# Optimization experiments

Hardware: AMD Instinct MI355X
Metric: run time of the kernel (lower is better)

The kernel has to match this reference:

```python
import jax, jax.numpy as jnp
from jax import lax
import numpy as np

N_E = 1024
E_DIM = 512
BETA = 0.25


def setup_inputs() -> dict:
    key = jax.random.key(0)
    k1, k2 = jax.random.split(key)
    z = jax.random.normal(k1, (16, 4096, E_DIM), dtype=jnp.float32)
    # torch init: uniform(-1/n_e, 1/n_e)
    codebook = jax.random.uniform(k2, (N_E, E_DIM), dtype=jnp.float32,
                                  minval=-1.0 / N_E, maxval=1.0 / N_E)
    return {"z": z, "codebook": codebook}


def reference(z, codebook):
    zf = z.reshape(-1, z.shape[-1])                      # (N, e_dim)
    # squared-distance matrix: ||z||^2 + ||e||^2 - 2 z e^T  -> (N, n_e)
    d = (jnp.sum(zf * zf, axis=1, keepdims=True)
         + jnp.sum(codebook * codebook, axis=1)
         - 2.0 * (zf @ codebook.T))
    idx = jnp.argmin(d, axis=1)                          # (N,)
    z_q = codebook[idx].reshape(z.shape)                 # (B, S, e_dim)
    loss = (jnp.mean((z_q - lax.stop_gradient(z)) ** 2)
            + BETA * jnp.mean((lax.stop_gradient(z_q) - z) ** 2))
    # straight-through estimator
    z_q_st = z + lax.stop_gradient(z_q - z)
    # perplexity of code usage (mean of one-hot == normalized counts)
    counts = jnp.zeros((codebook.shape[0],), dtype=z.dtype).at[idx].add(1.0)
    e_mean = counts / idx.shape[0]
    perplexity = jnp.exp(-jnp.sum(e_mean * jnp.log(e_mean + 1e-10)))
    return (loss, z_q_st, idx, perplexity)
```

## Files before the change

### kernel.cpp

```cpp
#include <hip/hip_runtime.h>
#include <hip/hip_bf16.h>

#define N_ROWS 65536
#define EDIM   512
#define NCODES 1024

#define WS_LOSS   0
#define WS_COUNTS 1
#define WS_ENORM  1025
#define WS_ZNORM  2049
#define WS_AMBCNT (2049 + 65536)
#define WS_WINNER (WS_AMBCNT + 1)
#define WS_AMBLST (WS_WINNER + 65536)
#define AMB_CAP   32768
#define WS_E2_OFF (1u << 20)
#define WS_FAST_BYTES (3u * 1024u * 1024u + 4096u)

#define AMB_EPS 1.6e-4f

typedef short short8 __attribute__((ext_vector_type(8)));
typedef float f32x4  __attribute__((ext_vector_type(4)));

#define AS1C(p) ((const __attribute__((address_space(1))) void*)(p))
#define AS3(p)  ((__attribute__((address_space(3))) void*)(p))

static __device__ __forceinline__ unsigned short f2bf(float f) {
    unsigned u = __float_as_uint(f);
    u += 0x7FFFu + ((u >> 16) & 1u);
    return (unsigned short)(u >> 16);
}
static __device__ __forceinline__ float bf2f(unsigned short h) {
    return __uint_as_float(((unsigned)h) << 16);
}

__global__ __launch_bounds__(256) void vq_prep(const float* __restrict__ cb,
                                               float* __restrict__ ws) {
    int j = blockIdx.x;
    int tid = threadIdx.x;
    float2 v = *(const float2*)&cb[(size_t)j * EDIM + tid * 2];
    float s = v.x * v.x + v.y * v.y;
    #pragma unroll
    for (int off = 32; off > 0; off >>= 1) s += __shfl_down(s, off);
    __shared__ float ls[4];
    int wave = tid >> 6, lane = tid & 63;
    if (lane == 0) ls[wave] = s;
    __syncthreads();
    if (tid == 0) {
        ws[WS_ENORM + j] = ls[0] + ls[1] + ls[2] + ls[3];
        ws[WS_COUNTS + j] = 0.0f;
        if (j == 0) {
            ws[WS_LOSS] = 0.0f;
            ((int*)ws)[WS_AMBCNT] = 0;
        }
    }
}

__global__ __launch_bounds__(256) void vq_znorm(const float* __restrict__ z,
                                                float* __restrict__ ws) {
    int tid  = threadIdx.x;
    int lrow = tid >> 5;
    int c    = tid & 31;
    long row = (long)blockIdx.x * 8 + lrow;
    const float* p = z + row * EDIM + (c >> 3) * 128 + (c & 7);
    float r = p[0] * p[0];
    #pragma unroll
    for (int i = 1; i < 16; ++i) {
        float v = p[i * 8];
        r += v * v;
    }
    r += __shfl_xor(r, 1);
    r += __shfl_xor(r, 2);
    r += __shfl_xor(r, 4);
    r += __shfl_xor(r, 8);
    r += __shfl_xor(r, 16);
    if (c == 0) ws[WS_ZNORM + row] = r;
}

__global__ __launch_bounds__(256) void vq_convz(const float* __restrict__ z,
                                                unsigned short* __restrict__ z2) {
    const int tid = threadIdx.x;
    const int p = blockIdx.x;
    const long row0 = (long)p * 128;
    const int row = tid >> 1, half = tid & 1;
    for (int kc = 0; kc < 16; ++kc) {
        const float* src = z + (row0 + row) * EDIM + kc * 32 + half * 16;
        float f[16];
        #pragma unroll
        for (int q = 0; q < 4; ++q) {
            float4 v = ((const float4*)src)[q];
            f[q*4+0] = v.x; f[q*4+1] = v.y; f[q*4+2] = v.z; f[q*4+3] = v.w;
        }
        unsigned hi[8], lo[8];
        #pragma unroll
        for (int q = 0; q < 8; ++q) {
            unsigned short h0 = f2bf(f[2*q]);
            unsigned short h1 = f2bf(f[2*q+1]);
            unsigned short l0 = f2bf(f[2*q]   - bf2f(h0));
            unsigned short l1 = f2bf(f[2*q+1] - bf2f(h1));
            hi[q] = (unsigned)h0 | ((unsigned)h1 << 16);
            lo[q] = (unsigned)l0 | ((unsigned)l1 << 16);
        }
        size_t base = ((size_t)(p * 16 + kc) * 2) * 4096;
        unsigned* dhi = (unsigned*)(z2 + base        + row * 32 + half * 16);
        unsigned* dlo = (unsigned*)(z2 + base + 4096 + row * 32 + half * 16);
        ((uint4*)dhi)[0] = make_uint4(hi[0], hi[1], hi[2], hi[3]);
        ((uint4*)dhi)[1] = make_uint4(hi[4], hi[5], hi[6], hi[7]);
        ((uint4*)dlo)[0] = make_uint4(lo[0], lo[1], lo[2], lo[3]);
        ((uint4*)dlo)[1] = make_uint4(lo[4], lo[5], lo[6], lo[7]);
    }
}

__global__ __launch_bounds__(256) void vq_convcb(const float* __restrict__ cb,
                                                 unsigned short* __restrict__ e2) {
    const int tid = threadIdx.x;
    const int cc = blockIdx.x;
    const int row = tid >> 1, half = tid & 1;
    for (int kc = 0; kc < 16; ++kc) {
        const float* src = cb + (size_t)(cc * 128 + row) * EDIM + kc * 32 + half * 16;
        float f[16];
        #pragma unroll
        for (int q = 0; q < 4; ++q) {
            float4 v = ((const float4*)src)[q];
            f[q*4+0] = v.x; f[q*4+1] = v.y; f[q*4+2] = v.z; f[q*4+3] = v.w;
        }
        unsigned hi[8], lo[8];
        #pragma unroll
        for (int q = 0; q < 8; ++q) {
            unsigned short h0 = f2bf(f[2*q]);
            unsigned short h1 = f2bf(f[2*q+1]);
            unsigned short l0 = f2bf(f[2*q]   - bf2f(h0));
            unsigned short l1 = f2bf(f[2*q+1] - bf2f(h1));
            hi[q] = (unsigned)h0 | ((unsigned)h1 << 16);
            lo[q] = (unsigned)l0 | ((unsigned)l1 << 16);
        }
        size_t base = ((size_t)(cc * 16 + kc) * 2) * 4096;
        unsigned* dhi = (unsigned*)(e2 + base        + row * 32 + half * 16);
        unsigned* dlo = (unsigned*)(e2 + base + 4096 + row * 32 + half * 16);
        ((uint4*)dhi)[0] = make_uint4(hi[0], hi[1], hi[2], hi[3]);
        ((uint4*)dhi)[1] = make_uint4(hi[4], hi[5], hi[6], hi[7]);
        ((uint4*)dlo)[0] = make_uint4(lo[0], lo[1], lo[2], lo[3]);
        ((uint4*)dlo)[1] = make_uint4(lo[4], lo[5], lo[6], lo[7]);
    }
}

__global__ __launch_bounds__(256, 2) void vq_mfma(const unsigned short* __restrict__ z2,
                                                  const unsigned short* __restrict__ e2,
                                                  const float* __restrict__ ws,
                                                  int* __restrict__ winner,
                                                  int* __restrict__ amb_count,
                                                  int* __restrict__ amb_list) {
    __shared__ unsigned short stage[16384];
    __shared__ float fv1[2][128];
    __shared__ float fv2[2][128];
    __shared__ int   fc1[2][128];

    const int tid = threadIdx.x;
    const int lane = tid & 63, w = tid >> 6;
    const int rw = (w & 1) * 64, cw = (w >> 1) * 64;
    const int ml = lane & 15, kg = lane >> 4;
    const long row0 = (long)blockIdx.x * 128;
    const float* __restrict__ enorm = ws + WS_ENORM;

    float v1[16], v2[16];
    int   c1[16];
    #pragma unroll
    for (int i = 0; i < 16; ++i) { v1[i] = INFINITY; v2[i] = INFINITY; c1[i] = 0; }

    const unsigned short* zt = stage;
    const unsigned short* et = stage + 8192;

    for (int cc = 0; cc < 8; ++cc) {
        f32x4 acc[4][4];
        #pragma unroll
        for (int rt = 0; rt < 4; ++rt)
            #pragma unroll
            for (int ct = 0; ct < 4; ++ct)
                acc[rt][ct] = (f32x4){0.f, 0.f, 0.f, 0.f};

        for (int kc = 0; kc < 16; ++kc) {
            __syncthreads();
            const uint4* zsrc = (const uint4*)(z2 + (size_t)(blockIdx.x * 16 + kc) * 8192);
            const uint4* esrc = (const uint4*)(e2 + (size_t)(cc * 16 + kc) * 8192);
            uint4* st = (uint4*)stage;
#if defined(__has_builtin) && __has_builtin(__builtin_amdgcn_global_load_lds)
            #pragma unroll
            for (int it = 0; it < 4; ++it) {
                int base = it * 256 + w * 64;
                __builtin_amdgcn_global_load_lds(AS1C(zsrc + base + lane), AS3(st + base), 16, 0, 0);
            }
            #pragma unroll
            for (int it = 0; it < 4; ++it) {
                int base = it * 256 + w * 64;
                __builtin_amdgcn_global_load_lds(AS1C(esrc + base + lane), AS3(st + 1024 + base), 16, 0, 0);
            }
#else
            #pragma unroll
            for (int it = 0; it < 4; ++it) {
                int i = it * 256 + tid;
                st[i] = zsrc[i];
            }
            #pragma unroll
            for (int it = 0; it < 4; ++it) {
                int i = it * 256 + tid;
                st[1024 + i] = esrc[i];
            }
#endif
            __syncthreads();

            short8 a[4][2], b[4][2];
            #pragma unroll
            for (int rt = 0; rt < 4; ++rt) {
                a[rt][0] = *(const short8*)&zt[        (rw + rt * 16 + ml) * 32 + kg * 8];
                a[rt][1] = *(const short8*)&zt[4096 + (rw + rt * 16 + ml) * 32 + kg * 8];
            }
            #pragma unroll
            for (int ct = 0; ct < 4; ++ct) {
                b[ct][0] = *(const short8*)&et[        (cw + ct * 16 + ml) * 32 + kg * 8];
                b[ct][1] = *(const short8*)&et[4096 + (cw + ct * 16 + ml) * 32 + kg * 8];
            }
            #pragma unroll
            for (int rt = 0; rt < 4; ++rt)
                #pragma unroll
                for (int ct = 0; ct < 4; ++ct) {
                    acc[rt][ct] = __builtin_amdgcn_mfma_f32_16x16x32_bf16(a[rt][0], b[ct][0], acc[rt][ct], 0, 0, 0);
                    acc[rt][ct] = __builtin_amdgcn_mfma_f32_16x16x32_bf16(a[rt][0], b[ct][1], acc[rt][ct], 0, 0, 0);
                    acc[rt][ct] = __builtin_amdgcn_mfma_f32_16x16x32_bf16(a[rt][1], b[ct][0], acc[rt][ct], 0, 0, 0);
                }
        }

        float en[4];
        #pragma unroll
        for (int ct = 0; ct < 4; ++ct) en[ct] = enorm[cc * 128 + cw + ct * 16 + ml];
        #pragma unroll
        for (int rt = 0; rt < 4; ++rt)
            #pragma unroll
            for (int ct = 0; ct < 4; ++ct) {
                int code = cc * 128 + cw + ct * 16 + ml;
                #pragma unroll
                for (int reg = 0; reg < 4; ++reg) {
                    float d = fmaf(-2.0f, acc[rt][ct][reg], en[ct]);
                    int i = rt * 4 + reg;
                    bool lt1 = d < v1[i];
                    bool lt2 = d < v2[i];
                    v2[i] = lt1 ? v1[i] : (lt2 ? d : v2[i]);
                    v1[i] = lt1 ? d : v1[i];
                    c1[i] = lt1 ? code : c1[i];
                }
            }
    }

    #pragma unroll
    for (int i = 0; i < 16; ++i) {
        #pragma unroll
        for (int off = 1; off < 16; off <<= 1) {
            float ov1 = __shfl_xor(v1[i], off);
            int   oc1 = __shfl_xor(c1[i], off);
            float ov2 = __shfl_xor(v2[i], off);
            bool take = (ov1 < v1[i]) || (ov1 == v1[i] && oc1 < c1[i]);
            float nv2 = take ? fminf(v1[i], ov2) : fminf(v2[i], ov1);
            v1[i] = take ? ov1 : v1[i];
            c1[i] = take ? oc1 : c1[i];
            v2[i] = nv2;
        }
    }
    __syncthreads();
    if (ml == 0) {
        #pragma unroll
        for (int i = 0; i < 16; ++i) {
            int row = rw + (i >> 2) * 16 + kg * 4 + (i & 3);
            fv1[w >> 1][row] = v1[i];
            fv2[w >> 1][row] = v2[i];
            fc1[w >> 1][row] = c1[i];
        }
    }
    __syncthreads();
    if (tid < 128) {
        float a1 = fv1[0][tid], a2 = fv2[0][tid];
        int   ac = fc1[0][tid];
        float b1 = fv1[1][tid], b2 = fv2[1][tid];
        int   bc = fc1[1][tid];
        bool take = (b1 < a1) || (b1 == a1 && bc < ac);
        float V1 = take ? b1 : a1;
        int   C1 = take ? bc : ac;
        float V2 = take ? fminf(a1, b2) : fminf(a2, b1);
        winner[row0 + tid] = C1;
        if (V2 - V1 < AMB_EPS) {
            int p = atomicAdd(amb_count, 1);
            if (p < AMB_CAP) amb_list[p] = (int)(row0 + tid);
        }
    }
}

#define RB 8
#define ZSR 9
__global__ __launch_bounds__(256) void vq_recheck(const float* __restrict__ z,
                                                  const float* __restrict__ cb,
                                                  const float* __restrict__ ws,
                                                  int* __restrict__ winner,
                                                  const int* __restrict__ amb_count,
                                                  const int* __restrict__ amb_list) {
    __shared__ float zs[EDIM * ZSR];
    __shared__ float wred_d[4];
    __shared__ int   wred_i[4];
    const int tid = threadIdx.x;
    const int lane = tid & 63, wv = tid >> 6;
    const float* __restrict__ enorm = ws + WS_ENORM;

    int n = *amb_count;
    bool overflow = (n > AMB_CAP);
    if (overflow) n = N_ROWS;
    int nIter = (n + RB - 1) / RB;

    const float* ec[4];
    float en4[4];
    #pragma unroll
    for (int c = 0; c < 4; ++c) {
        ec[c]  = cb + (size_t)(tid + 256 * c) * EDIM;
        en4[c] = enorm[tid + 256 * c];
    }

    for (int ii = blockIdx.x; ii < nIter; ii += gridDim.x) {
        int rows[RB];
        #pragma unroll
        for (int j = 0; j < RB; ++j) {
            int idx = ii * RB + j;
            if (idx >= n) idx = n - 1;
            rows[j] = overflow ? idx : amb_list[idx];
        }
        __syncthreads();
        #pragma unroll
        for (int j = 0; j < RB; ++j) {
            float2 v = *(const float2*)&z[(long)rows[j] * EDIM + tid * 2];
            zs[(tid * 2 + 0) * ZSR + j] = v.x;
            zs[(tid * 2 + 1) * ZSR + j] = v.y;
        }
        __syncthreads();

        float acc[RB][4];
        #pragma unroll
        for (int r = 0; r < RB; ++r)
            #pragma unroll
            for (int c = 0; c < 4; ++c) acc[r][c] = 0.0f;

        for (int k0 = 0; k0 < EDIM; k0 += 32) {
            float ain[RB][4];
            #pragma unroll
            for (int r = 0; r < RB; ++r)
                #pragma unroll
                for (int c = 0; c < 4; ++c) ain[r][c] = 0.0f;
            #pragma unroll
            for (int ks = 0; ks < 32; ks += 8) {
                float er[4][8];
                #pragma unroll
                for (int c = 0; c < 4; ++c) {
                    float4 a = *(const float4*)&ec[c][k0 + ks];
                    float4 b = *(const float4*)&ec[c][k0 + ks + 4];
                    er[c][0]=a.x; er[c][1]=a.y; er[c][2]=a.z; er[c][3]=a.w;
                    er[c][4]=b.x; er[c][5]=b.y; er[c][6]=b.z; er[c][7]=b.w;
                }
                #pragma unroll
                for (int kk = 0; kk < 8; ++kk) {
                    const float* zp = &zs[(k0 + ks + kk) * ZSR];
                    float4 z0 = *(const float4*)zp;
                    float4 z1 = *(const float4*)(zp + 4);
                    float zr[RB] = {z0.x, z0.y, z0.z, z0.w, z1.x, z1.y, z1.z, z1.w};
                    #pragma unroll
                    for (int r = 0; r < RB; ++r)
                        #pragma unroll
                        for (int c = 0; c < 4; ++c)
                            ain[r][c] = fmaf(zr[r], er[c][kk], ain[r][c]);
                }
            }
            #pragma unroll
            for (int r = 0; r < RB; ++r)
                #pragma unroll
                for (int c = 0; c < 4; ++c) acc[r][c] += ain[r][c];
        }

        #pragma unroll
        for (int r = 0; r < RB; ++r) {
            float zn = ws[WS_ZNORM + rows[r]];
            float bd = INFINITY;
            int   bc = 0;
            #pragma unroll
            for (int c = 0; c < 4; ++c) {
                float t = zn + en4[c];
                float d = t - 2.0f * acc[r][c];
                if (d < bd) { bd = d; bc = tid + 256 * c; }
            }
            #pragma unroll
            for (int off = 1; off < 64; off <<= 1) {
                float od = __shfl_xor(bd, off);
                int   oi = __shfl_xor(bc, off);
                if (od < bd || (od == bd && oi < bc)) { bd = od; bc = oi; }
            }
            if (lane == 0) { wred_d[wv] = bd; wred_i[wv] = bc; }
            __syncthreads();
            if (tid == 0) {
                float fd = wred_d[0]; int fi = wred_i[0];
                #pragma unroll
                for (int t2 = 1; t2 < 4; ++t2) {
                    if (wred_d[t2] < fd || (wred_d[t2] == fd && wred_i[t2] < fi)) {
                        fd = wred_d[t2]; fi = wred_i[t2];
                    }
                }
                winner[rows[r]] = fi;
            }
            __syncthreads();
        }
    }
}

__global__ __launch_bounds__(256) void vq_emit(const float* __restrict__ z,
                                               const float* __restrict__ cb,
                                               const int* __restrict__ winner,
                                               float* __restrict__ ws,
                                               float* __restrict__ out_zq,
                                               float* __restrict__ out_idx) {
    __shared__ float lred[4];
    const int tid = threadIdx.x;
    const long row0 = (long)blockIdx.x * 128;
    if (tid < 128) {
        int wi = winner[row0 + tid];
        out_idx[row0 + tid] = (float)wi;
        atomicAdd(&ws[WS_COUNTS + wi], 1.0f);
    }
    float lsum = 0.0f;
    for (int r = 0; r < 128; ++r) {
        int wv = winner[row0 + r];
        float2 e  = *(const float2*)&cb[(size_t)wv * EDIM + tid * 2];
        float2 zz = *(const float2*)&z[(row0 + r) * EDIM + tid * 2];
        float d0 = e.x - zz.x, d1 = e.y - zz.y;
        float2 o; o.x = zz.x + d0; o.y = zz.y + d1;
        *(float2*)&out_zq[(row0 + r) * EDIM + tid * 2] = o;
        lsum = fmaf(d0, d0, fmaf(d1, d1, lsum));
    }
    #pragma unroll
    for (int off = 32; off > 0; off >>= 1) lsum += __shfl_down(lsum, off);
    int wave = tid >> 6, lane = tid & 63;
    if (lane == 0) lred[wave] = lsum;
    __syncthreads();
    if (tid == 0) atomicAdd(&ws[WS_LOSS], lred[0] + lred[1] + lred[2] + lred[3]);
}

__global__ __launch_bounds__(1024) void vq_final(const float* __restrict__ ws,
                                                 float* __restrict__ out,
                                                 long off_perp) {
    int tid = threadIdx.x;
    float c = ws[WS_COUNTS + tid] * (1.0f / (float)N_ROWS);
    float t = c * logf(c + 1e-10f);
    #pragma unroll
    for (int off = 32; off > 0; off >>= 1) t += __shfl_down(t, off);
    __shared__ float ls[16];
    int wave = tid >> 6, lane = tid & 63;
    if (lane == 0) ls[wave] = t;
    __syncthreads();
    if (tid == 0) {
        float h = 0.0f;
        #pragma unroll
        for (int i = 0; i < 16; ++i) h += ls[i];
        out[off_perp] = expf(-h);
        out[0] = ws[WS_LOSS] * 1.25f / (float)((long)N_ROWS * EDIM);
    }
}

#define ROWS_PER_BLOCK 128
#define CODE_CHUNK     64
#define KCHUNK         32
#define ZSTRIDE        132
#define ESTRIDE        68

__global__ __launch_bounds__(256) void vq_main_fb(const float* __restrict__ z,
                                                  const float* __restrict__ cb,
                                                  float* __restrict__ ws,
                                                  float* __restrict__ out_zq,
                                                  float* __restrict__ out_idx) {
    __shared__ float zt[KCHUNK * ZSTRIDE];
    __shared__ float et[KCHUNK * ESTRIDE];
    __shared__ float red_d[ROWS_PER_BLOCK * 8];
    __shared__ int   red_i[ROWS_PER_BLOCK * 8];
    __shared__ int   winner[ROWS_PER_BLOCK];
    __shared__ float lred[4];

    const int tid = threadIdx.x;
    const int tx = tid & 7;
    const int ty = tid >> 3;
    const long row0 = (long)blockIdx.x * ROWS_PER_BLOCK;
    const float* __restrict__ enorm = ws + WS_ENORM;
    const float* __restrict__ znorm = ws + WS_ZNORM;

    float zn[4];
    #pragma unroll
    for (int i = 0; i < 4; ++i) zn[i] = znorm[row0 + ty * 4 + i];

    float best[4];
    int   bidx[4];
    #pragma unroll
    for (int i = 0; i < 4; ++i) { best[i] = INFINITY; bidx[i] = 0; }

    const int kq    = (tid & 7) * 4;
    const int rbase = tid >> 3;

    for (int c = 0; c < NCODES; c += CODE_CHUNK) {
        float acc[4][8];
        #pragma unroll
        for (int i = 0; i < 4; ++i)
            #pragma unroll
            for (int j = 0; j < 8; ++j) acc[i][j] = 0.0f;

        for (int k0 = 0; k0 < EDIM; k0 += KCHUNK) {
            __syncthreads();
            #pragma unroll
            for (int it = 0; it < 4; ++it) {
                int r = rbase + it * 32;
                float4 v = *(const float4*)&z[(row0 + r) * EDIM + k0 + kq];
                zt[(kq + 0) * ZSTRIDE + r] = v.x;
                zt[(kq + 1) * ZSTRIDE + r] = v.y;
                zt[(kq + 2) * ZSTRIDE + r] = v.z;
                zt[(kq + 3) * ZSTRIDE + r] = v.w;
            }
            #pragma unroll
            for (int it = 0; it < 2; ++it) {
                int e = rbase + it * 32;
                float4 v = *(const float4*)&cb[(size_t)(c + e) * EDIM + k0 + kq];
                et[(kq + 0) * ESTRIDE + e] = v.x;
                et[(kq + 1) * ESTRIDE + e] = v.y;
                et[(kq + 2) * ESTRIDE + e] = v.z;
                et[(kq + 3) * ESTRIDE + e] = v.w;
            }
            __syncthreads();
            float ain[4][8];
            #pragma unroll
            for (int i = 0; i < 4; ++i)
                #pragma unroll
                for (int j = 0; j < 8; ++j) ain[i][j] = 0.0f;
            #pragma unroll
            for (int kk = 0; kk < KCHUNK; ++kk) {
                float4 zv = *(const float4*)&zt[kk * ZSTRIDE + ty * 4];
                float4 e0 = *(const float4*)&et[kk * ESTRIDE + tx * 8];
                float4 e1 = *(const float4*)&et[kk * ESTRIDE + tx * 8 + 4];
                float za[4] = {zv.x, zv.y, zv.z, zv.w};
                float ea[8] = {e0.x, e0.y, e0.z, e0.w, e1.x, e1.y, e1.z, e1.w};
                #pragma unroll
                for (int i = 0; i < 4; ++i)
                    #pragma unroll
                    for (int j = 0; j < 8; ++j)
                        ain[i][j] = fmaf(za[i], ea[j], ain[i][j]);
            }
            #pragma unroll
            for (int i = 0; i < 4; ++i)
                #pragma unroll
                for (int j = 0; j < 8; ++j) acc[i][j] += ain[i][j];
        }
        #pragma unroll
        for (int j = 0; j < 8; ++j) {
            int code = c + tx * 8 + j;
            float en = enorm[code];
            #pragma unroll
            for (int i = 0; i < 4; ++i) {
                float t = zn[i] + en;
                float d = t - 2.0f * acc[i][j];
                if (d < best[i]) { best[i] = d; bidx[i] = code; }
            }
        }
    }

    __syncthreads();
    #pragma unroll
    for (int i = 0; i < 4; ++i) {
        red_d[(ty * 4 + i) * 8 + tx] = best[i];
        red_i[(ty * 4 + i) * 8 + tx] = bidx[i];
    }
    __syncthreads();
    if (tid < ROWS_PER_BLOCK) {
        float bd = red_d[tid * 8];
        int   bi = red_i[tid * 8];
        #pragma unroll
        for (int t = 1; t < 8; ++t) {
            float dv = red_d[tid * 8 + t];
            int   iv = red_i[tid * 8 + t];
            if (dv < bd || (dv == bd && iv < bi)) { bd = dv; bi = iv; }
        }
        winner[tid] = bi;
        out_idx[row0 + tid] = (float)bi;
        atomicAdd(&ws[WS_COUNTS + bi], 1.0f);
    }
    __syncthreads();

    float lsum = 0.0f;
    for (int r = 0; r < ROWS_PER_BLOCK; ++r) {
        int w = winner[r];
        float2 e  = *(const float2*)&cb[(size_t)w * EDIM + tid * 2];
        float2 zz = *(const float2*)&z[(row0 + r) * EDIM + tid * 2];
        float d0 = e.x - zz.x, d1 = e.y - zz.y;
        float2 o; o.x = zz.x + d0; o.y = zz.y + d1;
        *(float2*)&out_zq[(row0 + r) * EDIM + tid * 2] = o;
        lsum = fmaf(d0, d0, fmaf(d1, d1, lsum));
    }
    #pragma unroll
    for (int off = 32; off > 0; off >>= 1) lsum += __shfl_down(lsum, off);
    int wave = tid >> 6, lane = tid & 63;
    if (lane == 0) lred[wave] = lsum;
    __syncthreads();
    if (tid == 0) atomicAdd(&ws[WS_LOSS], lred[0] + lred[1] + lred[2] + lred[3]);
}

extern "C" void kernel_launch(void* const* d_in, const int* in_sizes, int n_in,
                              void* d_out, int out_size, void* d_ws, size_t ws_size,
                              hipStream_t stream) {
    const float* z  = (const float*)d_in[0];
    const float* cb = (const float*)d_in[1];
    float* out = (float*)d_out;
    float* ws  = (float*)d_ws;

    float* out_zq  = out + 1;
    float* out_idx = out + 1 + (long)N_ROWS * EDIM;
    long   off_perp = 1 + (long)N_ROWS * EDIM + N_ROWS;

    hipLaunchKernelGGL(vq_prep, dim3(NCODES), dim3(256), 0, stream, cb, ws);
    hipLaunchKernelGGL(vq_znorm, dim3(N_ROWS / 8), dim3(256), 0, stream, z, ws);

    if (ws_size >= (size_t)WS_FAST_BYTES) {
        unsigned short* z2 = (unsigned short*)(out + 4);
        unsigned short* e2 = (unsigned short*)((char*)d_ws + WS_E2_OFF);
        int* winner    = ((int*)ws) + WS_WINNER;
        int* amb_count = ((int*)ws) + WS_AMBCNT;
        int* amb_list  = ((int*)ws) + WS_AMBLST;

        hipLaunchKernelGGL(vq_convz, dim3(N_ROWS / 128), dim3(256), 0, stream, z, z2);
        hipLaunchKernelGGL(vq_convcb, dim3(8), dim3(256), 0, stream, cb, e2);
        hipLaunchKernelGGL(vq_mfma, dim3(N_ROWS / 128), dim3(256), 0, stream,
                           z2, e2, ws, winner, amb_count, amb_list);
        hipLaunchKernelGGL(vq_recheck, dim3(512), dim3(256), 0, stream,
                           z, cb, ws, winner, amb_count, amb_list);
        hipLaunchKernelGGL(vq_emit, dim3(N_ROWS / 128), dim3(256), 0, stream,
                           z, cb, winner, ws, out_zq, out_idx);
    } else {
        hipLaunchKernelGGL(vq_main_fb, dim3(N_ROWS / 128), dim3(256), 0, stream,
                           z, cb, ws, out_zq, out_idx);
    }
    hipLaunchKernelGGL(vq_final, dim3(1), dim3(1024), 0, stream, ws, out, off_perp);
}
```

Baseline: 696.9 us.

## Double-buffer MFMA tiles with 512-thread blocks covering 256 codes per pass

```diff
diff --git a/kernel.cpp b/kernel.cpp
--- a/kernel.cpp
+++ b/kernel.cpp
@@ -143,33 +143,56 @@
     }
 }
 
-__global__ __launch_bounds__(256, 2) void vq_mfma(const unsigned short* __restrict__ z2,
+__device__ __forceinline__ void stage48(const char* zs, const char* es0, const char* es1,
+                                        char* db, int tid, int w) {
+    const int t16 = tid << 4;
+    const int wb  = w << 10;
+    __builtin_amdgcn_global_load_lds(AS1C(zs + t16),         AS3(db + wb),          16, 0, 0);
+    __builtin_amdgcn_global_load_lds(AS1C(zs + 8192 + t16),  AS3(db + 8192 + wb),   16, 0, 0);
+    __builtin_amdgcn_global_load_lds(AS1C(es0 + t16),        AS3(db + 16384 + wb),  16, 0, 0);
+    __builtin_amdgcn_global_load_lds(AS1C(es0 + 8192 + t16), AS3(db + 24576 + wb),  16, 0, 0);
+    __builtin_amdgcn_global_load_lds(AS1C(es1 + t16),        AS3(db + 32768 + wb),  16, 0, 0);
+    __builtin_amdgcn_global_load_lds(AS1C(es1 + 8192 + t16), AS3(db + 40960 + wb),  16, 0, 0);
+}
+
+__global__ __launch_bounds__(512, 2) void vq_mfma(const unsigned short* __restrict__ z2,
                                                   const unsigned short* __restrict__ e2,
                                                   const float* __restrict__ ws,
                                                   int* __restrict__ winner,
                                                   int* __restrict__ amb_count,
                                                   int* __restrict__ amb_list) {
-    __shared__ unsigned short stage[16384];
-    __shared__ float fv1[2][128];
-    __shared__ float fv2[2][128];
-    __shared__ int   fc1[2][128];
-
-    const int tid = threadIdx.x;
+    __shared__ __attribute__((aligned(16))) char sb[2][49152];
+    __shared__ float enorm_lds[NCODES];
+    __shared__ float fv1[4][128];
+    __shared__ float fv2[4][128];
+    __shared__ int   fc1[4][128];
+
+    const int tid  = threadIdx.x;
     const int lane = tid & 63, w = tid >> 6;
-    const int rw = (w & 1) * 64, cw = (w >> 1) * 64;
+    const int rw   = (w & 1) * 64;
+    const int wcol = w >> 1;
+    const int cw   = wcol * 64;
     const int ml = lane & 15, kg = lane >> 4;
     const long row0 = (long)blockIdx.x * 128;
-    const float* __restrict__ enorm = ws + WS_ENORM;
+
+    enorm_lds[tid]       = ws[WS_ENORM + tid];
+    enorm_lds[tid + 512] = ws[WS_ENORM + tid + 512];
 
     float v1[16], v2[16];
     int   c1[16];
     #pragma unroll
     for (int i = 0; i < 16; ++i) { v1[i] = INFINITY; v2[i] = INFINITY; c1[i] = 0; }
 
-    const unsigned short* zt = stage;
-    const unsigned short* et = stage + 8192;
-
-    for (int cc = 0; cc < 8; ++cc) {
+    const size_t zpan = (size_t)blockIdx.x * 16 * 8192;
+
+    stage48((const char*)(z2 + zpan),
+            (const char*)e2,
+            (const char*)(e2 + (size_t)16 * 8192),
+            sb[0], tid, w);
+    __syncthreads();
+
+    int cur = 0;
+    for (int p = 0; p < 4; ++p) {
         f32x4 acc[4][4];
         #pragma unroll
         for (int rt = 0; rt < 4; ++rt)
@@ -177,36 +200,18 @@
             for (int ct = 0; ct < 4; ++ct)
                 acc[rt][ct] = (f32x4){0.f, 0.f, 0.f, 0.f};
 
+        #pragma unroll 2
         for (int kc = 0; kc < 16; ++kc) {
-            __syncthreads();
-            const uint4* zsrc = (const uint4*)(z2 + (size_t)(blockIdx.x * 16 + kc) * 8192);
-            const uint4* esrc = (const uint4*)(e2 + (size_t)(cc * 16 + kc) * 8192);
-            uint4* st = (uint4*)stage;
-#if defined(__has_builtin) && __has_builtin(__builtin_amdgcn_global_load_lds)
-            #pragma unroll
-            for (int it = 0; it < 4; ++it) {
-                int base = it * 256 + w * 64;
-                __builtin_amdgcn_global_load_lds(AS1C(zsrc + base + lane), AS3(st + base), 16, 0, 0);
-            }
-            #pragma unroll
-            for (int it = 0; it < 4; ++it) {
-                int base = it * 256 + w * 64;
-                __builtin_amdgcn_global_load_lds(AS1C(esrc + base + lane), AS3(st + 1024 + base), 16, 0, 0);
-            }
-#else
-            #pragma unroll
-            for (int it = 0; it < 4; ++it) {
-                int i = it * 256 + tid;
-                st[i] = zsrc[i];
-            }
-            #pragma unroll
-            for (int it = 0; it < 4; ++it) {
-                int i = it * 256 + tid;
-                st[1024 + i] = esrc[i];
-            }
-#endif
-            __syncthreads();
-
+            const int s = p * 16 + kc;
+            if (s + 1 < 64) {
+                const int s2 = s + 1, p2 = s2 >> 4, kc2 = s2 & 15;
+                const char* zs  = (const char*)(z2 + zpan + (size_t)kc2 * 8192);
+                const char* es0 = (const char*)(e2 + ((size_t)(2 * p2)     * 16 + kc2) * 8192);
+                const char* es1 = (const char*)(e2 + ((size_t)(2 * p2 + 1) * 16 + kc2) * 8192);
+                stage48(zs, es0, es1, sb[cur ^ 1], tid, w);
+            }
+            const unsigned short* zt = (const unsigned short*)sb[cur];
+            const unsigned short* et = (const unsigned short*)(sb[cur] + 16384);
             short8 a[4][2], b[4][2];
             #pragma unroll
             for (int rt = 0; rt < 4; ++rt) {
@@ -215,8 +220,10 @@
             }
             #pragma unroll
             for (int ct = 0; ct < 4; ++ct) {
-                b[ct][0] = *(const short8*)&et[        (cw + ct * 16 + ml) * 32 + kg * 8];
-                b[ct][1] = *(const short8*)&et[4096 + (cw + ct * 16 + ml) * 32 + kg * 8];
+                const int c2  = cw + ct * 16 + ml;
+                const int off = (c2 >> 7) * 8192 + (c2 & 127) * 32 + kg * 8;
+                b[ct][0] = *(const short8*)&et[off];
+                b[ct][1] = *(const short8*)&et[off + 4096];
             }
             #pragma unroll
             for (int rt = 0; rt < 4; ++rt)
@@ -226,19 +233,21 @@
                     acc[rt][ct] = __builtin_amdgcn_mfma_f32_16x16x32_bf16(a[rt][0], b[ct][1], acc[rt][ct], 0, 0, 0);
                     acc[rt][ct] = __builtin_amdgcn_mfma_f32_16x16x32_bf16(a[rt][1], b[ct][0], acc[rt][ct], 0, 0, 0);
                 }
-        }
-
-        float en[4];
-        #pragma unroll
-        for (int ct = 0; ct < 4; ++ct) en[ct] = enorm[cc * 128 + cw + ct * 16 + ml];
-        #pragma unroll
-        for (int rt = 0; rt < 4; ++rt)
-            #pragma unroll
-            for (int ct = 0; ct < 4; ++ct) {
-                int code = cc * 128 + cw + ct * 16 + ml;
+            asm volatile("s_waitcnt vmcnt(0)" ::: "memory");
+            __builtin_amdgcn_s_barrier();
+            asm volatile("" ::: "memory");
+            cur ^= 1;
+        }
+
+        #pragma unroll
+        for (int ct = 0; ct < 4; ++ct) {
+            const int code = p * 256 + cw + ct * 16 + ml;
+            const float en = enorm_lds[code];
+            #pragma unroll
+            for (int rt = 0; rt < 4; ++rt)
                 #pragma unroll
                 for (int reg = 0; reg < 4; ++reg) {
-                    float d = fmaf(-2.0f, acc[rt][ct][reg], en[ct]);
+                    float d = fmaf(-2.0f, acc[rt][ct][reg], en);
                     int i = rt * 4 + reg;
                     bool lt1 = d < v1[i];
                     bool lt2 = d < v2[i];
@@ -246,7 +255,7 @@
                     v1[i] = lt1 ? d : v1[i];
                     c1[i] = lt1 ? code : c1[i];
                 }
-            }
+        }
     }
 
     #pragma unroll
@@ -268,25 +277,29 @@
         #pragma unroll
         for (int i = 0; i < 16; ++i) {
             int row = rw + (i >> 2) * 16 + kg * 4 + (i & 3);
-            fv1[w >> 1][row] = v1[i];
-            fv2[w >> 1][row] = v2[i];
-            fc1[w >> 1][row] = c1[i];
+            fv1[wcol][row] = v1[i];
+            fv2[wcol][row] = v2[i];
+            fc1[wcol][row] = c1[i];
         }
     }
     __syncthreads();
     if (tid < 128) {
-        float a1 = fv1[0][tid], a2 = fv2[0][tid];
-        int   ac = fc1[0][tid];
-        float b1 = fv1[1][tid], b2 = fv2[1][tid];
-        int   bc = fc1[1][tid];
-        bool take = (b1 < a1) || (b1 == a1 && bc < ac);
-        float V1 = take ? b1 : a1;
-        int   C1 = take ? bc : ac;
-        float V2 = take ? fminf(a1, b2) : fminf(a2, b1);
+        float V1 = fv1[0][tid], V2 = fv2[0][tid];
+        int   C1 = fc1[0][tid];
+        #pragma unroll
+        for (int g = 1; g < 4; ++g) {
+            float b1 = fv1[g][tid], b2 = fv2[g][tid];
+            int   bc = fc1[g][tid];
+            bool take = (b1 < V1) || (b1 == V1 && bc < C1);
+            float nv2 = take ? fminf(V1, b2) : fminf(V2, b1);
+            V1 = take ? b1 : V1;
+            C1 = take ? bc : C1;
+            V2 = nv2;
+        }
         winner[row0 + tid] = C1;
         if (V2 - V1 < AMB_EPS) {
-            int p = atomicAdd(amb_count, 1);
-            if (p < AMB_CAP) amb_list[p] = (int)(row0 + tid);
+            int pq = atomicAdd(amb_count, 1);
+            if (pq < AMB_CAP) amb_list[pq] = (int)(row0 + tid);
         }
     }
 }
@@ -629,7 +642,7 @@
 
         hipLaunchKernelGGL(vq_convz, dim3(N_ROWS / 128), dim3(256), 0, stream, z, z2);
         hipLaunchKernelGGL(vq_convcb, dim3(8), dim3(256), 0, stream, cb, e2);
-        hipLaunchKernelGGL(vq_mfma, dim3(N_ROWS / 128), dim3(256), 0, stream,
+        hipLaunchKernelGGL(vq_mfma, dim3(N_ROWS / 128), dim3(512), 0, stream,
                            z2, e2, ws, winner, amb_count, amb_list);
         hipLaunchKernelGGL(vq_recheck, dim3(512), dim3(256), 0, stream,
                            z, cb, ws, winner, amb_count, amb_list);
```

New measurement: 749.4 us. 7.5% more time.

## Double-buffer swizzled LDS staging in the MFMA distance kernel

Applied to the files above, without the earlier changes.

```diff
diff --git a/kernel.cpp b/kernel.cpp
--- a/kernel.cpp
+++ b/kernel.cpp
@@ -143,110 +143,128 @@
     }
 }
 
+__device__ __forceinline__ void stage32(const char* zs, const char* es,
+                                        char* db, int goff, int w) {
+    const int wb = w << 10;
+    #pragma unroll
+    for (int i = 0; i < 4; ++i) {
+        __builtin_amdgcn_global_load_lds(AS1C(zs + goff + i * 2048),
+                                         AS3(db + i * 4096 + wb), 16, 0, 0);
+        __builtin_amdgcn_global_load_lds(AS1C(es + goff + i * 2048),
+                                         AS3(db + 16384 + i * 4096 + wb), 16, 0, 0);
+    }
+}
+
 __global__ __launch_bounds__(256, 2) void vq_mfma(const unsigned short* __restrict__ z2,
                                                   const unsigned short* __restrict__ e2,
                                                   const float* __restrict__ ws,
                                                   int* __restrict__ winner,
                                                   int* __restrict__ amb_count,
                                                   int* __restrict__ amb_list) {
-    __shared__ unsigned short stage[16384];
+    __shared__ __attribute__((aligned(16))) char sb[2][32768];
+    __shared__ float enorm_lds[NCODES];
     __shared__ float fv1[2][128];
     __shared__ float fv2[2][128];
     __shared__ int   fc1[2][128];
 
-    const int tid = threadIdx.x;
+    const int tid  = threadIdx.x;
     const int lane = tid & 63, w = tid >> 6;
-    const int rw = (w & 1) * 64, cw = (w >> 1) * 64;
+    const int rw   = (w & 1) * 64;
+    const int wcol = w >> 1;
+    const int cw   = wcol * 64;
     const int ml = lane & 15, kg = lane >> 4;
     const long row0 = (long)blockIdx.x * 128;
-    const float* __restrict__ enorm = ws + WS_ENORM;
+
+    const int t3 = tid >> 3;
+    const int sl = (tid & 7) ^ (t3 & 7);
+    const int goff = t3 * 64 + (sl & 3) * 16 + (sl >> 2) * 8192;
+
+    const int xr = ml & 7;
+    const int o0 = (kg ^ xr) * 16;
+    const int o1 = ((4 + kg) ^ xr) * 16;
+    const int za = (rw + ml) * 128;
+    const int ea = 16384 + (cw + ml) * 128;
+
+    #pragma unroll
+    for (int i = 0; i < 4; ++i) enorm_lds[tid + i * 256] = ws[WS_ENORM + tid + i * 256];
 
     float v1[16], v2[16];
     int   c1[16];
     #pragma unroll
     for (int i = 0; i < 16; ++i) { v1[i] = INFINITY; v2[i] = INFINITY; c1[i] = 0; }
 
-    const unsigned short* zt = stage;
-    const unsigned short* et = stage + 8192;
-
-    for (int cc = 0; cc < 8; ++cc) {
-        f32x4 acc[4][4];
+    const char* z2b = (const char*)z2 + (size_t)blockIdx.x * 16 * 16384;
+    const char* e2b = (const char*)e2;
+
+    f32x4 acc[4][4];
+    #pragma unroll
+    for (int rt = 0; rt < 4; ++rt)
+        #pragma unroll
+        for (int ct = 0; ct < 4; ++ct)
+            acc[rt][ct] = (f32x4){0.f, 0.f, 0.f, 0.f};
+
+    stage32(z2b, e2b, sb[0], goff, w);
+    __syncthreads();
+
+    int cur = 0;
+    #pragma unroll 2
+    for (int s = 0; s < 128; ++s) {
+        if (s + 1 < 128) {
+            const int s2 = s + 1;
+            stage32(z2b + (size_t)(s2 & 15) * 16384,
+                    e2b + (size_t)s2 * 16384,
+                    sb[cur ^ 1], goff, w);
+        }
+        const char* bz = sb[cur];
+        short8 a[4][2], b[4][2];
+        #pragma unroll
+        for (int rt = 0; rt < 4; ++rt) {
+            a[rt][0] = *(const short8*)(bz + za + rt * 2048 + o0);
+            a[rt][1] = *(const short8*)(bz + za + rt * 2048 + o1);
+        }
+        #pragma unroll
+        for (int ct = 0; ct < 4; ++ct) {
+            b[ct][0] = *(const short8*)(bz + ea + ct * 2048 + o0);
+            b[ct][1] = *(const short8*)(bz + ea + ct * 2048 + o1);
+        }
         #pragma unroll
         for (int rt = 0; rt < 4; ++rt)
             #pragma unroll
-            for (int ct = 0; ct < 4; ++ct)
-                acc[rt][ct] = (f32x4){0.f, 0.f, 0.f, 0.f};
-
-        for (int kc = 0; kc < 16; ++kc) {
-            __syncthreads();
-            const uint4* zsrc = (const uint4*)(z2 + (size_t)(blockIdx.x * 16 + kc) * 8192);
-            const uint4* esrc = (const uint4*)(e2 + (size_t)(cc * 16 + kc) * 8192);
-            uint4* st = (uint4*)stage;
-#if defined(__has_builtin) && __has_builtin(__builtin_amdgcn_global_load_lds)
-            #pragma unroll
-            for (int it = 0; it < 4; ++it) {
-                int base = it * 256 + w * 64;
-                __builtin_amdgcn_global_load_lds(AS1C(zsrc + base + lane), AS3(st + base), 16, 0, 0);
-            }
-            #pragma unroll
-            for (int it = 0; it < 4; ++it) {
-                int base = it * 256 + w * 64;
-                __builtin_amdgcn_global_load_lds(AS1C(esrc + base + lane), AS3(st + 1024 + base), 16, 0, 0);
-            }
-#else
-            #pragma unroll
-            for (int it = 0; it < 4; ++it) {
-                int i = it * 256 + tid;
-                st[i] = zsrc[i];
-            }
-            #pragma unroll
-            for (int it = 0; it < 4; ++it) {
-                int i = it * 256 + tid;
-                st[1024 + i] = esrc[i];
-            }
-#endif
-            __syncthreads();
-
-            short8 a[4][2], b[4][2];
-            #pragma unroll
-            for (int rt = 0; rt < 4; ++rt) {
-                a[rt][0] = *(const short8*)&zt[        (rw + rt * 16 + ml) * 32 + kg * 8];
-                a[rt][1] = *(const short8*)&zt[4096 + (rw + rt * 16 + ml) * 32 + kg * 8];
-            }
-            #pragma unroll
             for (int ct = 0; ct < 4; ++ct) {
-                b[ct][0] = *(const short8*)&et[        (cw + ct * 16 + ml) * 32 + kg * 8];
-                b[ct][1] = *(const short8*)&et[4096 + (cw + ct * 16 + ml) * 32 + kg * 8];
+                acc[rt][ct] = __builtin_amdgcn_mfma_f32_16x16x32_bf16(a[rt][0], b[ct][0], acc[rt][ct], 0, 0, 0);
+                acc[rt][ct] = __builtin_amdgcn_mfma_f32_16x16x32_bf16(a[rt][0], b[ct][1], acc[rt][ct], 0, 0, 0);
+                acc[rt][ct] = __builtin_amdgcn_mfma_f32_16x16x32_bf16(a[rt][1], b[ct][0], acc[rt][ct], 0, 0, 0);
+            }
+        asm volatile("s_waitcnt vmcnt(0)" ::: "memory");
+        __builtin_amdgcn_s_barrier();
+        asm volatile("" ::: "memory");
+        cur ^= 1;
+
+        if ((s & 15) == 15) {
+            const int cc = s >> 4;
+            #pragma unroll
+            for (int ct = 0; ct < 4; ++ct) {
+                const int code = cc * 128 + cw + ct * 16 + ml;
+                const float en = enorm_lds[code];
+                #pragma unroll
+                for (int rt = 0; rt < 4; ++rt)
+                    #pragma unroll
+                    for (int reg = 0; reg < 4; ++reg) {
+                        float d = fmaf(-2.0f, acc[rt][ct][reg], en);
+                        int i = rt * 4 + reg;
+                        bool lt1 = d < v1[i];
+                        bool lt2 = d < v2[i];
+                        v2[i] = lt1 ? v1[i] : (lt2 ? d : v2[i]);
+                        v1[i] = lt1 ? d : v1[i];
+                        c1[i] = lt1 ? code : c1[i];
+                    }
             }
             #pragma unroll
             for (int rt = 0; rt < 4; ++rt)
                 #pragma unroll
-                for (int ct = 0; ct < 4; ++ct) {
-                    acc[rt][ct] = __builtin_amdgcn_mfma_f32_16x16x32_bf16(a[rt][0], b[ct][0], acc[rt][ct], 0, 0, 0);
-                    acc[rt][ct] = __builtin_amdgcn_mfma_f32_16x16x32_bf16(a[rt][0], b[ct][1], acc[rt][ct], 0, 0, 0);
-                    acc[rt][ct] = __builtin_amdgcn_mfma_f32_16x16x32_bf16(a[rt][1], b[ct][0], acc[rt][ct], 0, 0, 0);
-                }
-        }
-
-        float en[4];
-        #pragma unroll
-        for (int ct = 0; ct < 4; ++ct) en[ct] = enorm[cc * 128 + cw + ct * 16 + ml];
-        #pragma unroll
-        for (int rt = 0; rt < 4; ++rt)
-            #pragma unroll
-            for (int ct = 0; ct < 4; ++ct) {
-                int code = cc * 128 + cw + ct * 16 + ml;
-                #pragma unroll
-                for (int reg = 0; reg < 4; ++reg) {
-                    float d = fmaf(-2.0f, acc[rt][ct][reg], en[ct]);
-                    int i = rt * 4 + reg;
-                    bool lt1 = d < v1[i];
-                    bool lt2 = d < v2[i];
-                    v2[i] = lt1 ? v1[i] : (lt2 ? d : v2[i]);
-                    v1[i] = lt1 ? d : v1[i];
-                    c1[i] = lt1 ? code : c1[i];
-                }
-            }
+                for (int ct = 0; ct < 4; ++ct)
+                    acc[rt][ct] = (f32x4){0.f, 0.f, 0.f, 0.f};
+        }
     }
 
     #pragma unroll
@@ -268,9 +286,9 @@
         #pragma unroll
         for (int i = 0; i < 16; ++i) {
             int row = rw + (i >> 2) * 16 + kg * 4 + (i & 3);
-            fv1[w >> 1][row] = v1[i];
-            fv2[w >> 1][row] = v2[i];
-            fc1[w >> 1][row] = c1[i];
+            fv1[wcol][row] = v1[i];
+            fv2[wcol][row] = v2[i];
+            fc1[wcol][row] = c1[i];
         }
     }
     __syncthreads();
@@ -631,7 +649,7 @@
         hipLaunchKernelGGL(vq_convcb, dim3(8), dim3(256), 0, stream, cb, e2);
         hipLaunchKernelGGL(vq_mfma, dim3(N_ROWS / 128), dim3(256), 0, stream,
                            z2, e2, ws, winner, amb_count, amb_list);
-        hipLaunchKernelGGL(vq_recheck, dim3(512), dim3(256), 0, stream,
+        hipLaunchKernelGGL(vq_recheck, dim3(1024), dim3(256), 0, stream,
                            z, cb, ws, winner, amb_count, amb_list);
         hipLaunchKernelGGL(vq_emit, dim3(N_ROWS / 128), dim3(256), 0, stream,
                            z, cb, winner, ws, out_zq, out_idx);
```

Result: slower. 713.7 us (+2.4%).
